# Kernel tuning notes

Measured on AMD Instinct MI355X. Metric: run time of the kernel, lower is better.

The kernel has to match this reference:

```python
import jax, jax.numpy as jnp
import numpy as np

B, K, L = 8, 288, 16384   # K = C*kh*kw = 32*3*3
O = 64                    # output channels


def setup_inputs() -> dict:
    key = jax.random.key(0)
    k1, k2, k3 = jax.random.split(key, 3)
    x_unf = jax.random.normal(k1, (B, K, L), dtype=jnp.float32)
    w = jax.random.normal(k2, (O, 32, 3, 3), dtype=jnp.float32)
    b = jax.random.normal(k3, (O,), dtype=jnp.float32)
    gamma = jnp.float32(0.005)
    return {"x_unf": x_unf, "w": w, "b": b, "gamma": gamma}


def reference(x_unf, w, b, gamma):
    # torch: l = x_unf.transpose(1,2)[:,:,:,None] - w.view(1,1,-1,w.size(0))
    #        l = sum(l**2, dim=2); t = exp(-gamma*l) + b
    o = w.shape[0]
    wv = jnp.reshape(w, (-1,))            # row-major flatten, same as torch .view
    wv = jnp.reshape(wv, (-1, o))         # [K, O] (memory reinterpretation, NOT transpose)
    xt = jnp.transpose(x_unf, (0, 2, 1))  # [B, L, K]
    x2 = jnp.sum(xt * xt, axis=-1, keepdims=True)       # [B, L, 1]
    w2 = jnp.sum(wv * wv, axis=0)[None, None, :]        # [1, 1, O]
    xw = jnp.einsum('blk,ko->blo', xt, wv)              # [B, L, O]
    d2 = x2 + w2 - 2.0 * xw                             # [B, L, O]
    t = jnp.exp(-gamma * d2)
    return t + b
```

## Files before the change

### kernel.cpp

```cpp
#include <hip/hip_runtime.h>

#define LDIM 16384
#define KDIM 288
#define ODIM 64
#define BDIM 8

typedef float f32x4 __attribute__((ext_vector_type(4)));
typedef short bf16x8 __attribute__((ext_vector_type(8)));

__device__ __forceinline__ short f2bf(float f) {
  unsigned u = __builtin_bit_cast(unsigned, f);
  unsigned r = u + 0x7FFFu + ((u >> 16) & 1u);
  return (short)(r >> 16);
}

__global__ __launch_bounds__(256) void gauss_pre(const float* __restrict__ w,
                                                 const float* __restrict__ gammap,
                                                 short* __restrict__ wfrag,
                                                 float* __restrict__ cw) {
  int tid = threadIdx.x;

  for (int f = tid; f < 9 * 256; f += 256) {
    int ln = f & 63;
    int nt = (f >> 6) & 3;
    int kc = f >> 8;
    int k0 = kc * 32 + (ln >> 4) * 8;
    int n = nt * 16 + (ln & 15);
    bf16x8 v;
#pragma unroll
    for (int j = 0; j < 8; ++j) v[j] = f2bf(w[(k0 + j) * 64 + n]);
    *(bf16x8*)(wfrag + f * 8) = v;
  }

  __shared__ float red[256];
  int o = tid & 63;
  int seg = tid >> 6;
  float s = 0.f;
#pragma unroll 4
  for (int k = seg * 72; k < seg * 72 + 72; ++k) {
    float v = w[k * 64 + o];
    s += v * v;
  }
  red[tid] = s;
  __syncthreads();
  if (tid < 64) {
    float t = red[tid] + red[tid + 64] + red[tid + 128] + red[tid + 192];
    cw[tid] = -gammap[0] * t;
  }
}

__global__ __launch_bounds__(256, 4) void gauss_main(
    const float* __restrict__ x, const short* __restrict__ wfrag,
    const float* __restrict__ cw, const float* __restrict__ bias,
    const float* __restrict__ gammap, float* __restrict__ out) {
  const int tid = threadIdx.x;
  const int lane = tid & 63;
  const int wvid = tid >> 6;
  const int m = lane & 15;
  const int quad = lane >> 4;

  const long g0 = (long)blockIdx.x * 128;
  const int bidx = (int)(g0 >> 14);
  const int l0 = (int)(g0 & (LDIM - 1));

  const float gamma = gammap[0];

  const float* xbase = x + (long)bidx * ((long)KDIM * LDIM) + (l0 + wvid * 32 + m);

  const f32x4 zero = {0.f, 0.f, 0.f, 0.f};
  f32x4 acc[2][4];
#pragma unroll
  for (int t = 0; t < 2; ++t)
#pragma unroll
    for (int nt = 0; nt < 4; ++nt) acc[t][nt] = zero;
  float s2[2] = {0.f, 0.f};

#pragma unroll 1
  for (int kc = 0; kc < 9; ++kc) {
    bf16x8 bfr[4];
    const short* wp = wfrag + ((kc * 4) * 64 + lane) * 8;
#pragma unroll
    for (int nt = 0; nt < 4; ++nt) bfr[nt] = *(const bf16x8*)(wp + nt * 512);

#pragma unroll
    for (int t = 0; t < 2; ++t) {
      const float* p = xbase + t * 16 + (long)(kc * 32 + quad * 8) * LDIM;
      float a[8];
#pragma unroll
      for (int j = 0; j < 8; ++j) a[j] = p[(long)j * LDIM];
      bf16x8 afr;
#pragma unroll
      for (int j = 0; j < 8; ++j) {
        s2[t] += a[j] * a[j];
        afr[j] = f2bf(a[j]);
      }
#pragma unroll
      for (int nt = 0; nt < 4; ++nt)
        acc[t][nt] =
            __builtin_amdgcn_mfma_f32_16x16x32_bf16(afr, bfr[nt], acc[t][nt], 0, 0, 0);
    }
  }

#pragma unroll
  for (int t = 0; t < 2; ++t) {
    s2[t] += __shfl_xor(s2[t], 16, 64);
    s2[t] += __shfl_xor(s2[t], 32, 64);
  }

  float cwv[4], bv[4];
#pragma unroll
  for (int nt = 0; nt < 4; ++nt) {
    int col = nt * 16 + m;
    cwv[nt] = cw[col];
    bv[nt] = bias[col];
  }

  const float coef = 2.f * gamma;
#pragma unroll
  for (int t = 0; t < 2; ++t) {
#pragma unroll
    for (int r = 0; r < 4; ++r) {
      int row = quad * 4 + r;
      float x2v = __shfl(s2[t], (lane & 48) | row, 64);
      float cx = -gamma * x2v;
      long grow = g0 + wvid * 32 + t * 16 + row;
      float* po = out + grow * 64 + m;
#pragma unroll
      for (int nt = 0; nt < 4; ++nt) {
        float e = coef * acc[t][nt][r] + (cx + cwv[nt]);
        po[nt * 16] = __expf(e) + bv[nt];
      }
    }
  }
}

extern "C" void kernel_launch(void* const* d_in, const int* in_sizes, int n_in,
                              void* d_out, int out_size, void* d_ws, size_t ws_size,
                              hipStream_t stream) {
  const float* x = (const float*)d_in[0];
  const float* w = (const float*)d_in[1];
  const float* b = (const float*)d_in[2];
  const float* gamma = (const float*)d_in[3];
  float* out = (float*)d_out;

  short* wfrag = (short*)d_ws;
  float* cw = (float*)((char*)d_ws + 36864);

  gauss_pre<<<1, 256, 0, stream>>>(w, gamma, wfrag, cw);
  gauss_main<<<1024, 256, 0, stream>>>(x, wfrag, cw, b, gamma, out);
}
```

Before: 241.9 us.

## Stage x tiles through double-buffered LDS with float4 loads; parallelize weight prep

The main kernel now loads each 32-row K chunk of x with coalesced float4 global loads into a padded, double-buffered shared-memory tile. It prefetches the next chunk into registers while MFMAs run on the current one, replacing strided scalar global loads per lane. The weight preprocessing kernel is split across 10 blocks instead of one serial block. The cost is 33 KB of LDS per block plus a barrier every iteration, which may reduce occupancy below the launch-bounds target.

Result: no change. 245.3 us (+1.4%).

```diff
diff --git a/kernel.cpp b/kernel.cpp
--- a/kernel.cpp
+++ b/kernel.cpp
@@ -4,6 +4,9 @@
 #define KDIM 288
 #define ODIM 64
 #define BDIM 8
+
+#define MT 128
+#define LPAD 132
 
 typedef float f32x4 __attribute__((ext_vector_type(4)));
 typedef short bf16x8 __attribute__((ext_vector_type(8)));
@@ -19,33 +22,34 @@
                                                  short* __restrict__ wfrag,
                                                  float* __restrict__ cw) {
   int tid = threadIdx.x;
+  int blk = blockIdx.x;
 
-  for (int f = tid; f < 9 * 256; f += 256) {
-    int ln = f & 63;
-    int nt = (f >> 6) & 3;
-    int kc = f >> 8;
+  if (blk < 9) {
+    int kc = blk;
+    int ln = tid & 63;
+    int nt = tid >> 6;
     int k0 = kc * 32 + (ln >> 4) * 8;
     int n = nt * 16 + (ln & 15);
     bf16x8 v;
 #pragma unroll
     for (int j = 0; j < 8; ++j) v[j] = f2bf(w[(k0 + j) * 64 + n]);
-    *(bf16x8*)(wfrag + f * 8) = v;
-  }
-
-  __shared__ float red[256];
-  int o = tid & 63;
-  int seg = tid >> 6;
-  float s = 0.f;
-#pragma unroll 4
-  for (int k = seg * 72; k < seg * 72 + 72; ++k) {
-    float v = w[k * 64 + o];
-    s += v * v;
-  }
-  red[tid] = s;
-  __syncthreads();
-  if (tid < 64) {
-    float t = red[tid] + red[tid + 64] + red[tid + 128] + red[tid + 192];
-    cw[tid] = -gammap[0] * t;
+    *(bf16x8*)(wfrag + ((kc * 4 + nt) * 64 + ln) * 8) = v;
+  } else {
+    __shared__ float red[256];
+    int o = tid & 63;
+    int seg = tid >> 6;
+    float s = 0.f;
+#pragma unroll 8
+    for (int k = seg * 72; k < seg * 72 + 72; ++k) {
+      float v = w[k * 64 + o];
+      s += v * v;
+    }
+    red[tid] = s;
+    __syncthreads();
+    if (tid < 64) {
+      float t = red[tid] + red[tid + 64] + red[tid + 128] + red[tid + 192];
+      cw[tid] = -gammap[0] * t;
+    }
   }
 }
 
@@ -53,19 +57,22 @@
     const float* __restrict__ x, const short* __restrict__ wfrag,
     const float* __restrict__ cw, const float* __restrict__ bias,
     const float* __restrict__ gammap, float* __restrict__ out) {
+  __shared__ float abuf[2][32 * LPAD];
+
   const int tid = threadIdx.x;
   const int lane = tid & 63;
   const int wvid = tid >> 6;
   const int m = lane & 15;
   const int quad = lane >> 4;
 
-  const long g0 = (long)blockIdx.x * 128;
+  const long g0 = (long)blockIdx.x * MT;
   const int bidx = (int)(g0 >> 14);
   const int l0 = (int)(g0 & (LDIM - 1));
 
-  const float gamma = gammap[0];
+  const float* xb = x + (long)bidx * ((long)KDIM * LDIM) + l0;
 
-  const float* xbase = x + (long)bidx * ((long)KDIM * LDIM) + (l0 + wvid * 32 + m);
+  const int srow0 = tid >> 5;
+  const int scol = (tid & 31) * 4;
 
   const f32x4 zero = {0.f, 0.f, 0.f, 0.f};
   f32x4 acc[2][4];
@@ -75,8 +82,32 @@
     for (int nt = 0; nt < 4; ++nt) acc[t][nt] = zero;
   float s2[2] = {0.f, 0.f};
 
+  float4 rs[4];
+#pragma unroll
+  for (int i = 0; i < 4; ++i) {
+    int row = srow0 + i * 8;
+    rs[i] = *(const float4*)(xb + (long)row * LDIM + scol);
+  }
+#pragma unroll
+  for (int i = 0; i < 4; ++i) {
+    int row = srow0 + i * 8;
+    *(float4*)&abuf[0][row * LPAD + scol] = rs[i];
+  }
+  __syncthreads();
+
 #pragma unroll 1
   for (int kc = 0; kc < 9; ++kc) {
+    const int pb = kc & 1;
+
+    if (kc < 8) {
+      const float* xn = xb + (long)((kc + 1) * 32) * LDIM;
+#pragma unroll
+      for (int i = 0; i < 4; ++i) {
+        int row = srow0 + i * 8;
+        rs[i] = *(const float4*)(xn + (long)row * LDIM + scol);
+      }
+    }
+
     bf16x8 bfr[4];
     const short* wp = wfrag + ((kc * 4) * 64 + lane) * 8;
 #pragma unroll
@@ -84,10 +115,10 @@
 
 #pragma unroll
     for (int t = 0; t < 2; ++t) {
-      const float* p = xbase + t * 16 + (long)(kc * 32 + quad * 8) * LDIM;
+      const float* ap = &abuf[pb][(quad * 8) * LPAD + wvid * 32 + t * 16 + m];
       float a[8];
 #pragma unroll
-      for (int j = 0; j < 8; ++j) a[j] = p[(long)j * LDIM];
+      for (int j = 0; j < 8; ++j) a[j] = ap[j * LPAD];
       bf16x8 afr;
 #pragma unroll
       for (int j = 0; j < 8; ++j) {
@@ -99,6 +130,15 @@
         acc[t][nt] =
             __builtin_amdgcn_mfma_f32_16x16x32_bf16(afr, bfr[nt], acc[t][nt], 0, 0, 0);
     }
+
+    if (kc < 8) {
+#pragma unroll
+      for (int i = 0; i < 4; ++i) {
+        int row = srow0 + i * 8;
+        *(float4*)&abuf[pb ^ 1][row * LPAD + scol] = rs[i];
+      }
+    }
+    __syncthreads();
   }
 
 #pragma unroll
@@ -107,6 +147,7 @@
     s2[t] += __shfl_xor(s2[t], 32, 64);
   }
 
+  const float gamma = gammap[0];
   float cwv[4], bv[4];
 #pragma unroll
   for (int nt = 0; nt < 4; ++nt) {
@@ -146,6 +187,6 @@
   short* wfrag = (short*)d_ws;
   float* cw = (float*)((char*)d_ws + 36864);
 
-  gauss_pre<<<1, 256, 0, stream>>>(w, gamma, wfrag, cw);
+  gauss_pre<<<10, 256, 0, stream>>>(w, gamma, wfrag, cw);
   gauss_main<<<1024, 256, 0, stream>>>(x, wfrag, cw, b, gamma, out);
 }
```

## Double-buffer x tiles via global_load_lds and stage output through LDS

Applied to the files above, without the earlier changes.

The main kernel now streams each 32-row K-chunk of x into a double-buffered LDS tile with direct global-to-LDS loads, prefetching two chunks ahead, instead of issuing strided per-lane global loads. Results are written to LDS first and then stored as coalesced 16-byte vectors. The weight preprocessing kernel is split across 10 blocks so it no longer runs serially in one block. This adds 32KB of LDS per block and extra barriers, which may reduce occupancy.

New measurement: 230.0 us. -4.9%, faster.

```diff
diff --git a/kernel.cpp b/kernel.cpp
--- a/kernel.cpp
+++ b/kernel.cpp
@@ -19,33 +19,34 @@
                                                  short* __restrict__ wfrag,
                                                  float* __restrict__ cw) {
   int tid = threadIdx.x;
+  int blk = blockIdx.x;
 
-  for (int f = tid; f < 9 * 256; f += 256) {
-    int ln = f & 63;
-    int nt = (f >> 6) & 3;
-    int kc = f >> 8;
+  if (blk < 9) {
+    int kc = blk;
+    int ln = tid & 63;
+    int nt = tid >> 6;
     int k0 = kc * 32 + (ln >> 4) * 8;
     int n = nt * 16 + (ln & 15);
     bf16x8 v;
 #pragma unroll
     for (int j = 0; j < 8; ++j) v[j] = f2bf(w[(k0 + j) * 64 + n]);
-    *(bf16x8*)(wfrag + f * 8) = v;
-  }
-
-  __shared__ float red[256];
-  int o = tid & 63;
-  int seg = tid >> 6;
-  float s = 0.f;
-#pragma unroll 4
-  for (int k = seg * 72; k < seg * 72 + 72; ++k) {
-    float v = w[k * 64 + o];
-    s += v * v;
-  }
-  red[tid] = s;
-  __syncthreads();
-  if (tid < 64) {
-    float t = red[tid] + red[tid + 64] + red[tid + 128] + red[tid + 192];
-    cw[tid] = -gammap[0] * t;
+    *(bf16x8*)(wfrag + ((kc * 4 + nt) * 64 + ln) * 8) = v;
+  } else {
+    __shared__ float red[256];
+    int o = tid & 63;
+    int seg = tid >> 6;
+    float s = 0.f;
+#pragma unroll 8
+    for (int k = seg * 72; k < seg * 72 + 72; ++k) {
+      float v = w[k * 64 + o];
+      s += v * v;
+    }
+    red[tid] = s;
+    __syncthreads();
+    if (tid < 64) {
+      float t = red[tid] + red[tid + 64] + red[tid + 128] + red[tid + 192];
+      cw[tid] = -gammap[0] * t;
+    }
   }
 }
 
@@ -53,6 +54,8 @@
     const float* __restrict__ x, const short* __restrict__ wfrag,
     const float* __restrict__ cw, const float* __restrict__ bias,
     const float* __restrict__ gammap, float* __restrict__ out) {
+  __shared__ float abuf[2][32 * 128];
+
   const int tid = threadIdx.x;
   const int lane = tid & 63;
   const int wvid = tid >> 6;
@@ -63,9 +66,23 @@
   const int bidx = (int)(g0 >> 14);
   const int l0 = (int)(g0 & (LDIM - 1));
 
-  const float gamma = gammap[0];
+  const float* xb = x + (long)bidx * ((long)KDIM * LDIM) + l0;
 
-  const float* xbase = x + (long)bidx * ((long)KDIM * LDIM) + (l0 + wvid * 32 + m);
+  const int srow = (lane >> 5);
+  const int scolf = (lane & 31) * 4;
+
+#define STAGE(KC, BUF)                                                         \
+  {                                                                            \
+    const float* xsrc = xb + (long)((KC) * 32) * LDIM;                         \
+    _Pragma("unroll") for (int i = 0; i < 4; ++i) {                            \
+      int s = wvid * 4 + i;                                                    \
+      const float* gp = xsrc + (long)(2 * s + srow) * LDIM + scolf;            \
+      __builtin_amdgcn_global_load_lds(                                        \
+          (const __attribute__((address_space(1))) unsigned int*)(void*)gp,    \
+          (__attribute__((address_space(3))) unsigned int*)&abuf[BUF][s * 256],\
+          16, 0, 0);                                                           \
+    }                                                                          \
+  }
 
   const f32x4 zero = {0.f, 0.f, 0.f, 0.f};
   f32x4 acc[2][4];
@@ -75,8 +92,14 @@
     for (int nt = 0; nt < 4; ++nt) acc[t][nt] = zero;
   float s2[2] = {0.f, 0.f};
 
+  STAGE(0, 0)
+  STAGE(1, 1)
+  __syncthreads();
+
 #pragma unroll 1
   for (int kc = 0; kc < 9; ++kc) {
+    const int pb = kc & 1;
+
     bf16x8 bfr[4];
     const short* wp = wfrag + ((kc * 4) * 64 + lane) * 8;
 #pragma unroll
@@ -84,10 +107,10 @@
 
 #pragma unroll
     for (int t = 0; t < 2; ++t) {
-      const float* p = xbase + t * 16 + (long)(kc * 32 + quad * 8) * LDIM;
+      const float* ap = &abuf[pb][(quad * 8) * 128 + wvid * 32 + t * 16 + m];
       float a[8];
 #pragma unroll
-      for (int j = 0; j < 8; ++j) a[j] = p[(long)j * LDIM];
+      for (int j = 0; j < 8; ++j) a[j] = ap[j * 128];
       bf16x8 afr;
 #pragma unroll
       for (int j = 0; j < 8; ++j) {
@@ -99,6 +122,9 @@
         acc[t][nt] =
             __builtin_amdgcn_mfma_f32_16x16x32_bf16(afr, bfr[nt], acc[t][nt], 0, 0, 0);
     }
+
+    __syncthreads();
+    if (kc < 7) STAGE(kc + 2, pb)
   }
 
 #pragma unroll
@@ -107,6 +133,7 @@
     s2[t] += __shfl_xor(s2[t], 32, 64);
   }
 
+  const float gamma = gammap[0];
   float cwv[4], bv[4];
 #pragma unroll
   for (int nt = 0; nt < 4; ++nt) {
@@ -115,6 +142,7 @@
     bv[nt] = bias[col];
   }
 
+  float* ob = &abuf[0][0] + wvid * 2048;
   const float coef = 2.f * gamma;
 #pragma unroll
   for (int t = 0; t < 2; ++t) {
@@ -123,14 +151,21 @@
       int row = quad * 4 + r;
       float x2v = __shfl(s2[t], (lane & 48) | row, 64);
       float cx = -gamma * x2v;
-      long grow = g0 + wvid * 32 + t * 16 + row;
-      float* po = out + grow * 64 + m;
+      int lr = t * 16 + row;
 #pragma unroll
       for (int nt = 0; nt < 4; ++nt) {
         float e = coef * acc[t][nt][r] + (cx + cwv[nt]);
-        po[nt * 16] = __expf(e) + bv[nt];
+        ob[lr * 64 + nt * 16 + m] = __expf(e) + bv[nt];
       }
     }
+  }
+  __syncthreads();
+
+  float* outw = out + (g0 + wvid * 32) * 64;
+#pragma unroll
+  for (int j = 0; j < 8; ++j) {
+    f32x4 v = *(f32x4*)&ob[j * 256 + lane * 4];
+    *(f32x4*)(outw + (j * 4 + (lane >> 4)) * 64 + (lane & 15) * 4) = v;
   }
 }
 
@@ -146,6 +181,6 @@
   short* wfrag = (short*)d_ws;
   float* cw = (float*)((char*)d_ws + 36864);
 
-  gauss_pre<<<1, 256, 0, stream>>>(w, gamma, wfrag, cw);
+  gauss_pre<<<10, 256, 0, stream>>>(w, gamma, wfrag, cw);
   gauss_main<<<1024, 256, 0, stream>>>(x, wfrag, cw, b, gamma, out);
 }
```
